# Kernel tuning notes

Measured on AMD Instinct MI355X. Metric: run time of the kernel, lower is better.

The kernel has to match this reference:

```python
import jax, jax.numpy as jnp
import numpy as np

H = 128
B = 512
T = 1024
FUT = 64


def setup_inputs() -> dict:
    key = jax.random.key(0)
    ks = jax.random.split(key, 11)
    k = 1.0 / np.sqrt(H)  # torch LSTMCell/Linear init range
    u = lambda kk, shape: jax.random.uniform(kk, shape, jnp.float32, -k, k)
    return {
        "x": jax.random.normal(ks[0], (B, T), jnp.float32),
        "W_ih1": u(ks[1], (4 * H, 1)),
        "b_ih1": u(ks[2], (4 * H,)),
        "W_hh1": u(ks[3], (4 * H, H)),
        "b_hh1": u(ks[4], (4 * H,)),
        "W_ih2": u(ks[5], (4 * H, H)),
        "b_ih2": u(ks[6], (4 * H,)),
        "W_hh2": u(ks[7], (4 * H, H)),
        "b_hh2": u(ks[8], (4 * H,)),
        "W_out": u(ks[9], (1, H)),
        "b_out": u(ks[10], (1,)),
        "future": FUT,
    }


def _cell(x_t, h, c, W_ih, b_ih, W_hh, b_hh):
    # torch.nn.LSTMCell: gates ordered i, f, g, o
    g = x_t @ W_ih.T + h @ W_hh.T + (b_ih + b_hh)
    i, f, gg, o = jnp.split(g, 4, axis=-1)
    c_new = jax.nn.sigmoid(f) * c + jax.nn.sigmoid(i) * jnp.tanh(gg)
    h_new = jax.nn.sigmoid(o) * jnp.tanh(c_new)
    return h_new, c_new


def reference(x, W_ih1, b_ih1, W_hh1, b_hh1, W_ih2, b_ih2, W_hh2, b_hh2, W_out, b_out, future):
    Bn = x.shape[0]
    Hn = W_hh1.shape[1]
    z = jnp.zeros((Bn, Hn), x.dtype)

    def enc_step(carry, x_t):
        h1, c1, h2, c2 = carry
        h1, c1 = _cell(x_t, h1, c1, W_ih1, b_ih1, W_hh1, b_hh1)
        h2, c2 = _cell(h1, h2, c2, W_ih2, b_ih2, W_hh2, b_hh2)
        return (h1, c1, h2, c2), None

    xs = x.T[:, :, None]  # [T, B, 1]
    (h1, c1, h2, c2), _ = jax.lax.scan(enc_step, (z, z, z, z), xs)
    out0 = h2 @ W_out.T + b_out  # [B, 1]

    def fut_step(carry, _):
        h1, c1, h2, c2, out = carry
        h1, c1 = _cell(out, h1, c1, W_ih1, b_ih1, W_hh1, b_hh1)
        h2, c2 = _cell(h1, h2, c2, W_ih2, b_ih2, W_hh2, b_hh2)
        out = h2 @ W_out.T + b_out
        return (h1, c1, h2, c2, out), out

    _, fouts = jax.lax.scan(fut_step, (h1, c1, h2, c2, out0), None, length=future - 1)
    # torch cats [B,1] tensors on dim=1 -> [B, future]
    return jnp.concatenate([out0, fouts[:, :, 0].T], axis=1)
```

## Files before the change

kernel.cpp:

```cpp
#include <hip/hip_runtime.h>

#define HH 128
#define TT 1024
#define NFUT 64
#define MB 2
#define NBLK 256
#define NITER (TT + NFUT - 1)

typedef _Float16 half8 __attribute__((ext_vector_type(8)));
typedef float floatx4 __attribute__((ext_vector_type(4)));

#define MFMA16(a, b, c) __builtin_amdgcn_mfma_f32_16x16x32_f16((a), (b), (c), 0, 0, 0)

__device__ __forceinline__ float sigm(float v) {
  return __builtin_amdgcn_rcpf(1.0f + __builtin_amdgcn_exp2f(v * -1.442695040888963f));
}
__device__ __forceinline__ float tanh_f(float v) {
  float a = __builtin_fabsf(v);
  float e = __builtin_amdgcn_exp2f(a * -2.885390081777927f);
  float r = (1.0f - e) * __builtin_amdgcn_rcpf(1.0f + e);
  return __builtin_copysignf(r, v);
}
__device__ __forceinline__ half8 ldw8(const float* __restrict__ p) {
  half8 r;
#pragma unroll
  for (int i = 0; i < 8; ++i) r[i] = (_Float16)p[i];
  return r;
}

__global__
__attribute__((amdgpu_flat_work_group_size(512, 512), amdgpu_waves_per_eu(2, 2)))
void lstm_kernel(
    const float* __restrict__ x,
    const float* __restrict__ W_ih1, const float* __restrict__ b_ih1,
    const float* __restrict__ W_hh1, const float* __restrict__ b_hh1,
    const float* __restrict__ W_ih2, const float* __restrict__ b_ih2,
    const float* __restrict__ W_hh2, const float* __restrict__ b_hh2,
    const float* __restrict__ W_out, const float* __restrict__ b_out,
    float* __restrict__ out)
{
  __shared__ __align__(16) _Float16 h1b[2][2048];
  __shared__ __align__(16) _Float16 h2b[2][2048];
  __shared__ __align__(16) _Float16 xs[TT * MB];
  __shared__ float opart[8 * MB];

  const int tid = (int)threadIdx.x;
  const int lane = tid & 63;
  const int w = tid >> 6;
  const int jl = lane & 15;
  const int rg = lane >> 4;
  const int j = w * 16 + jl;
  const int b0g = (int)blockIdx.x * MB;

  for (int idx = tid; idx < TT * MB; idx += 512) {
    int t = idx & (TT - 1);
    int bb = idx >> 10;
    xs[t * MB + bb] = (_Float16)x[(b0g + bb) * TT + t];
  }
  for (int idx = tid; idx < 2 * 2048; idx += 512) {
    h1b[idx >> 11][idx & 2047] = (_Float16)0.0f;
    h2b[idx >> 11][idx & 2047] = (_Float16)0.0f;
  }

  half8 A00, A01, A02, A03, A10, A11, A12, A13, A20, A21, A22, A23, A30, A31, A32, A33;
  half8 H00, H01, H02, H03, H10, H11, H12, H13, H20, H21, H22, H23, H30, H31, H32, H33;
  half8 I00, I01, I02, I03, I10, I11, I12, I13, I20, I21, I22, I23, I30, I31, I32, I33;
#define LDW(N, Q, P) do { \
    const float* _p = (P) + ((Q) * HH + j) * HH + rg * 8; \
    N##0 = ldw8(_p);      N##1 = ldw8(_p + 32); \
    N##2 = ldw8(_p + 64); N##3 = ldw8(_p + 96); } while (0)
  LDW(A0, 0, W_hh1); LDW(A1, 1, W_hh1); LDW(A2, 2, W_hh1); LDW(A3, 3, W_hh1);
  LDW(H0, 0, W_hh2); LDW(H1, 1, W_hh2); LDW(H2, 2, W_hh2); LDW(H3, 3, W_hh2);
  LDW(I0, 0, W_ih2); LDW(I1, 1, W_ih2); LDW(I2, 2, W_ih2); LDW(I3, 3, W_ih2);

  float bias1[4], bias2[4], wi1[4];
#pragma unroll
  for (int q = 0; q < 4; ++q) {
    bias1[q] = b_ih1[q * HH + j] + b_hh1[q * HH + j];
    bias2[q] = b_ih2[q * HH + j] + b_hh2[q * HH + j];
    wi1[q] = W_ih1[q * HH + j];
  }
  const float wo = W_out[j];
  const float bo = b_out[0];
  float c1a = 0.f, c1b = 0.f, c2a = 0.f, c2b = 0.f;

  __syncthreads();

  const int aoff = lane * 8;
  const int wb = ((j >> 5) << 9) + (((j >> 3) & 3) << 7) + (j & 7);

#define G1K(KF) do { \
    half8 av = *(const half8*)(&h1b[cur][KF * 512 + aoff]); \
    a0 = MFMA16(av, A0##KF, a0); a1 = MFMA16(av, A1##KF, a1); \
    a2 = MFMA16(av, A2##KF, a2); a3 = MFMA16(av, A3##KF, a3); } while (0)
#define G2K(KF) do { \
    half8 av = *(const half8*)(&h2b[cur][KF * 512 + aoff]); \
    g0 = MFMA16(av, H0##KF, g0); g1 = MFMA16(av, H1##KF, g1); \
    g2 = MFMA16(av, H2##KF, g2); g3 = MFMA16(av, H3##KF, g3); \
    half8 aw = *(const half8*)(&h1b[nxt][KF * 512 + aoff]); \
    g0 = MFMA16(aw, I0##KF, g0); g1 = MFMA16(aw, I1##KF, g1); \
    g2 = MFMA16(aw, I2##KF, g2); g3 = MFMA16(aw, I3##KF, g3); } while (0)

  for (int i = 0; i < NITER; ++i) {
    const int cur = i & 1;
    const int nxt = cur ^ 1;

    float x0, x1;
    if (i < TT) {
      x0 = (float)xs[i * MB + 0];
      x1 = (float)xs[i * MB + 1];
    } else {
      float s0 = bo, s1 = bo;
#pragma unroll
      for (int p = 0; p < 8; ++p) {
        s0 += opart[p * MB + 0];
        s1 += opart[p * MB + 1];
      }
      x0 = s0; x1 = s1;
    }

    floatx4 a0 = {0.f,0.f,0.f,0.f}, a1 = {0.f,0.f,0.f,0.f};
    floatx4 a2 = {0.f,0.f,0.f,0.f}, a3 = {0.f,0.f,0.f,0.f};
    G1K(0); G1K(1); G1K(2); G1K(3);
    {
      float gi0 = a0[0] + x0 * wi1[0] + bias1[0], gi1 = a0[1] + x1 * wi1[0] + bias1[0];
      float gf0 = a1[0] + x0 * wi1[1] + bias1[1], gf1 = a1[1] + x1 * wi1[1] + bias1[1];
      float gg0 = a2[0] + x0 * wi1[2] + bias1[2], gg1 = a2[1] + x1 * wi1[2] + bias1[2];
      float go0 = a3[0] + x0 * wi1[3] + bias1[3], go1 = a3[1] + x1 * wi1[3] + bias1[3];
      c1a = sigm(gf0) * c1a + sigm(gi0) * tanh_f(gg0);
      c1b = sigm(gf1) * c1b + sigm(gi1) * tanh_f(gg1);
      float h0 = sigm(go0) * tanh_f(c1a);
      float h1v = sigm(go1) * tanh_f(c1b);
      if (lane < 16) {
        h1b[nxt][wb] = (_Float16)h0;
        h1b[nxt][wb + 8] = (_Float16)h1v;
      }
    }
    __syncthreads();

    floatx4 g0 = {0.f,0.f,0.f,0.f}, g1 = {0.f,0.f,0.f,0.f};
    floatx4 g2 = {0.f,0.f,0.f,0.f}, g3 = {0.f,0.f,0.f,0.f};
    G2K(0); G2K(1); G2K(2); G2K(3);
    {
      float gi0 = g0[0] + bias2[0], gi1 = g0[1] + bias2[0];
      float gf0 = g1[0] + bias2[1], gf1 = g1[1] + bias2[1];
      float gg0 = g2[0] + bias2[2], gg1 = g2[1] + bias2[2];
      float go0 = g3[0] + bias2[3], go1 = g3[1] + bias2[3];
      c2a = sigm(gf0) * c2a + sigm(gi0) * tanh_f(gg0);
      c2b = sigm(gf1) * c2b + sigm(gi1) * tanh_f(gg1);
      float h0 = sigm(go0) * tanh_f(c2a);
      float h1v = sigm(go1) * tanh_f(c2b);
      if (lane < 16) {
        h2b[nxt][wb] = (_Float16)h0;
        h2b[nxt][wb + 8] = (_Float16)h1v;
      }
      if (i >= TT - 1) {
        float p0 = h0 * wo, p1 = h1v * wo;
        p0 += __shfl_xor(p0, 1); p1 += __shfl_xor(p1, 1);
        p0 += __shfl_xor(p0, 2); p1 += __shfl_xor(p1, 2);
        p0 += __shfl_xor(p0, 4); p1 += __shfl_xor(p1, 4);
        p0 += __shfl_xor(p0, 8); p1 += __shfl_xor(p1, 8);
        if (lane == 0) {
          opart[w * MB + 0] = p0;
          opart[w * MB + 1] = p1;
        }
      }
    }

    if (i >= TT - 1) {
      __syncthreads();
      if (w == 0 && lane < MB) {
        float s = bo;
#pragma unroll
        for (int p = 0; p < 8; ++p) s += opart[p * MB + lane];
        out[(b0g + lane) * NFUT + (i - (TT - 1))] = s;
      }
    }
    __builtin_amdgcn_sched_barrier(0);
  }
}

extern "C" void kernel_launch(void* const* d_in, const int* in_sizes, int n_in,
                              void* d_out, int out_size, void* d_ws, size_t ws_size,
                              hipStream_t stream) {
  const float* x     = (const float*)d_in[0];
  const float* W_ih1 = (const float*)d_in[1];
  const float* b_ih1 = (const float*)d_in[2];
  const float* W_hh1 = (const float*)d_in[3];
  const float* b_hh1 = (const float*)d_in[4];
  const float* W_ih2 = (const float*)d_in[5];
  const float* b_ih2 = (const float*)d_in[6];
  const float* W_hh2 = (const float*)d_in[7];
  const float* b_hh2 = (const float*)d_in[8];
  const float* W_out = (const float*)d_in[9];
  const float* b_out = (const float*)d_in[10];
  (void)in_sizes; (void)n_in; (void)out_size; (void)d_ws; (void)ws_size;

  lstm_kernel<<<dim3(NBLK), dim3(512), 0, stream>>>(
      x, W_ih1, b_ih1, W_hh1, b_hh1, W_ih2, b_ih2, W_hh2, b_hh2, W_out, b_out,
      (float*)d_out);
}
```

Before: 1.523 ms.

## Skew layer-2 of step t-1 with layer-1 of step t to halve barriers

Restructures the recurrence as a software pipeline. Each iteration computes layer 2 for the previous timestep and then layer 1 for the current timestep, both from the same previous buffers, so the encoder loop needs one barrier per iteration instead of two. Raises wave priority around the MFMA blocks and keeps x in fp32 in shared memory. In the future phase an extra barrier is still needed for the output feedback. The loop runs one more iteration, with edge guards at the first and last steps.

Result: slower. 1.582 ms (+3.9%).

```diff
diff --git a/kernel.cpp b/kernel.cpp
--- a/kernel.cpp
+++ b/kernel.cpp
@@ -5,7 +5,7 @@
 #define NFUT 64
 #define MB 2
 #define NBLK 256
-#define NITER (TT + NFUT - 1)
+#define NITER (TT + NFUT)
 
 typedef _Float16 half8 __attribute__((ext_vector_type(8)));
 typedef float floatx4 __attribute__((ext_vector_type(4)));
@@ -41,7 +41,7 @@
 {
   __shared__ __align__(16) _Float16 h1b[2][2048];
   __shared__ __align__(16) _Float16 h2b[2][2048];
-  __shared__ __align__(16) _Float16 xs[TT * MB];
+  __shared__ float xs[TT * MB];
   __shared__ float opart[8 * MB];
 
   const int tid = (int)threadIdx.x;
@@ -55,7 +55,7 @@
   for (int idx = tid; idx < TT * MB; idx += 512) {
     int t = idx & (TT - 1);
     int bb = idx >> 10;
-    xs[t * MB + bb] = (_Float16)x[(b0g + bb) * TT + t];
+    xs[t * MB + bb] = x[(b0g + bb) * TT + t];
   }
   for (int idx = tid; idx < 2 * 2048; idx += 512) {
     h1b[idx >> 11][idx & 2047] = (_Float16)0.0f;
@@ -89,73 +89,43 @@
   const int aoff = lane * 8;
   const int wb = ((j >> 5) << 9) + (((j >> 3) & 3) << 7) + (j & 7);
 
+#define G2K(KF) do { \
+    half8 bv = *(const half8*)(&h2b[prv][KF * 512 + aoff]); \
+    g0 = MFMA16(bv, H0##KF, g0); g1 = MFMA16(bv, H1##KF, g1); \
+    g2 = MFMA16(bv, H2##KF, g2); g3 = MFMA16(bv, H3##KF, g3); \
+    half8 aw = *(const half8*)(&h1b[prv][KF * 512 + aoff]); \
+    g0 = MFMA16(aw, I0##KF, g0); g1 = MFMA16(aw, I1##KF, g1); \
+    g2 = MFMA16(aw, I2##KF, g2); g3 = MFMA16(aw, I3##KF, g3); } while (0)
 #define G1K(KF) do { \
-    half8 av = *(const half8*)(&h1b[cur][KF * 512 + aoff]); \
+    half8 av = *(const half8*)(&h1b[prv][KF * 512 + aoff]); \
     a0 = MFMA16(av, A0##KF, a0); a1 = MFMA16(av, A1##KF, a1); \
     a2 = MFMA16(av, A2##KF, a2); a3 = MFMA16(av, A3##KF, a3); } while (0)
-#define G2K(KF) do { \
-    half8 av = *(const half8*)(&h2b[cur][KF * 512 + aoff]); \
-    g0 = MFMA16(av, H0##KF, g0); g1 = MFMA16(av, H1##KF, g1); \
-    g2 = MFMA16(av, H2##KF, g2); g3 = MFMA16(av, H3##KF, g3); \
-    half8 aw = *(const half8*)(&h1b[nxt][KF * 512 + aoff]); \
-    g0 = MFMA16(aw, I0##KF, g0); g1 = MFMA16(aw, I1##KF, g1); \
-    g2 = MFMA16(aw, I2##KF, g2); g3 = MFMA16(aw, I3##KF, g3); } while (0)
-
-  for (int i = 0; i < NITER; ++i) {
-    const int cur = i & 1;
-    const int nxt = cur ^ 1;
-
-    float x0, x1;
-    if (i < TT) {
-      x0 = (float)xs[i * MB + 0];
-      x1 = (float)xs[i * MB + 1];
-    } else {
-      float s0 = bo, s1 = bo;
-#pragma unroll
-      for (int p = 0; p < 8; ++p) {
-        s0 += opart[p * MB + 0];
-        s1 += opart[p * MB + 1];
-      }
-      x0 = s0; x1 = s1;
-    }
-
-    floatx4 a0 = {0.f,0.f,0.f,0.f}, a1 = {0.f,0.f,0.f,0.f};
-    floatx4 a2 = {0.f,0.f,0.f,0.f}, a3 = {0.f,0.f,0.f,0.f};
-    G1K(0); G1K(1); G1K(2); G1K(3);
-    {
-      float gi0 = a0[0] + x0 * wi1[0] + bias1[0], gi1 = a0[1] + x1 * wi1[0] + bias1[0];
-      float gf0 = a1[0] + x0 * wi1[1] + bias1[1], gf1 = a1[1] + x1 * wi1[1] + bias1[1];
-      float gg0 = a2[0] + x0 * wi1[2] + bias1[2], gg1 = a2[1] + x1 * wi1[2] + bias1[2];
-      float go0 = a3[0] + x0 * wi1[3] + bias1[3], go1 = a3[1] + x1 * wi1[3] + bias1[3];
-      c1a = sigm(gf0) * c1a + sigm(gi0) * tanh_f(gg0);
-      c1b = sigm(gf1) * c1b + sigm(gi1) * tanh_f(gg1);
-      float h0 = sigm(go0) * tanh_f(c1a);
-      float h1v = sigm(go1) * tanh_f(c1b);
-      if (lane < 16) {
-        h1b[nxt][wb] = (_Float16)h0;
-        h1b[nxt][wb + 8] = (_Float16)h1v;
-      }
-    }
-    __syncthreads();
+
+  for (int k = 0; k < NITER; ++k) {
+    const int cur = k & 1;
+    const int prv = cur ^ 1;
 
     floatx4 g0 = {0.f,0.f,0.f,0.f}, g1 = {0.f,0.f,0.f,0.f};
     floatx4 g2 = {0.f,0.f,0.f,0.f}, g3 = {0.f,0.f,0.f,0.f};
+    __builtin_amdgcn_s_setprio(1);
     G2K(0); G2K(1); G2K(2); G2K(3);
-    {
+    __builtin_amdgcn_s_setprio(0);
+
+    if (k >= 1) {
       float gi0 = g0[0] + bias2[0], gi1 = g0[1] + bias2[0];
       float gf0 = g1[0] + bias2[1], gf1 = g1[1] + bias2[1];
       float gg0 = g2[0] + bias2[2], gg1 = g2[1] + bias2[2];
       float go0 = g3[0] + bias2[3], go1 = g3[1] + bias2[3];
       c2a = sigm(gf0) * c2a + sigm(gi0) * tanh_f(gg0);
       c2b = sigm(gf1) * c2b + sigm(gi1) * tanh_f(gg1);
-      float h0 = sigm(go0) * tanh_f(c2a);
-      float h1v = sigm(go1) * tanh_f(c2b);
+      float h20 = sigm(go0) * tanh_f(c2a);
+      float h21 = sigm(go1) * tanh_f(c2b);
       if (lane < 16) {
-        h2b[nxt][wb] = (_Float16)h0;
-        h2b[nxt][wb + 8] = (_Float16)h1v;
-      }
-      if (i >= TT - 1) {
-        float p0 = h0 * wo, p1 = h1v * wo;
+        h2b[cur][wb] = (_Float16)h20;
+        h2b[cur][wb + 8] = (_Float16)h21;
+      }
+      if (k >= TT) {
+        float p0 = h20 * wo, p1 = h21 * wo;
         p0 += __shfl_xor(p0, 1); p1 += __shfl_xor(p1, 1);
         p0 += __shfl_xor(p0, 2); p1 += __shfl_xor(p1, 2);
         p0 += __shfl_xor(p0, 4); p1 += __shfl_xor(p1, 4);
@@ -167,15 +137,43 @@
       }
     }
 
-    if (i >= TT - 1) {
+    floatx4 a0 = {0.f,0.f,0.f,0.f}, a1 = {0.f,0.f,0.f,0.f};
+    floatx4 a2 = {0.f,0.f,0.f,0.f}, a3 = {0.f,0.f,0.f,0.f};
+    __builtin_amdgcn_s_setprio(1);
+    G1K(0); G1K(1); G1K(2); G1K(3);
+    __builtin_amdgcn_s_setprio(0);
+
+    float x0, x1;
+    if (k < TT) {
+      x0 = xs[k * MB + 0];
+      x1 = xs[k * MB + 1];
+    } else {
       __syncthreads();
-      if (w == 0 && lane < MB) {
-        float s = bo;
+      float s0 = bo, s1 = bo;
 #pragma unroll
-        for (int p = 0; p < 8; ++p) s += opart[p * MB + lane];
-        out[(b0g + lane) * NFUT + (i - (TT - 1))] = s;
-      }
+      for (int p = 0; p < 8; ++p) {
+        s0 += opart[p * MB + 0];
+        s1 += opart[p * MB + 1];
+      }
+      x0 = s0; x1 = s1;
+      if (w == 0 && lane < MB) out[(b0g + lane) * NFUT + (k - TT)] = (lane == 0) ? s0 : s1;
     }
+
+    if (k <= NITER - 2) {
+      float gi0 = a0[0] + x0 * wi1[0] + bias1[0], gi1 = a0[1] + x1 * wi1[0] + bias1[0];
+      float gf0 = a1[0] + x0 * wi1[1] + bias1[1], gf1 = a1[1] + x1 * wi1[1] + bias1[1];
+      float gg0 = a2[0] + x0 * wi1[2] + bias1[2], gg1 = a2[1] + x1 * wi1[2] + bias1[2];
+      float go0 = a3[0] + x0 * wi1[3] + bias1[3], go1 = a3[1] + x1 * wi1[3] + bias1[3];
+      c1a = sigm(gf0) * c1a + sigm(gi0) * tanh_f(gg0);
+      c1b = sigm(gf1) * c1b + sigm(gi1) * tanh_f(gg1);
+      float h10 = sigm(go0) * tanh_f(c1a);
+      float h11 = sigm(go1) * tanh_f(c1b);
+      if (lane < 16) {
+        h1b[cur][wb] = (_Float16)h10;
+        h1b[cur][wb + 8] = (_Float16)h11;
+      }
+    }
+    __syncthreads();
     __builtin_amdgcn_sched_barrier(0);
   }
 }
```
